# Kernel optimization log

Measured on AMD Instinct MI355X. Metric: run time of the kernel, lower is better.

Reference implementation:

```python
import jax, jax.numpy as jnp
import numpy as np

N_NODES = 200000
N_EDGES = 800000
N_MOL = 10000
IN_DIM, HDIM, EDGE_DIM = 40, 64, 16
BN_EPS = 1e-5


def _bn_eval(h, gamma, beta, mean, var):
    # BatchNorm1d in eval mode (running stats)
    return gamma * (h - mean) * jax.lax.rsqrt(var + BN_EPS) + beta


def _gine(x, src, dst, edge_attr, We, be, W, b, gamma, beta, mean, var):
    # GINEConv (eps=0): agg_i = sum_{(j->i)} relu(x_j + lin_e(e_ji)); h = nn(x + agg)
    msg = jax.nn.relu(x[src] + edge_attr @ We.T + be)          # [E, d]
    agg = jax.ops.segment_sum(msg, dst, num_segments=x.shape[0])
    h = (x + agg) @ W.T + b                                    # Linear
    h = _bn_eval(h, gamma, beta, mean, var)                    # BatchNorm1d
    return jax.nn.leaky_relu(h)                                # LeakyReLU(0.01); Dropout is identity in eval


def setup_inputs() -> dict:
    key = jax.random.key(0)
    ks = jax.random.split(key, 40)
    d = {}
    d['x'] = jax.random.normal(ks[0], (N_NODES, IN_DIM), jnp.float32)
    d['edge_index'] = jax.random.randint(ks[1], (2, N_EDGES), 0, N_NODES, jnp.int32)
    d['edge_attr'] = jax.random.normal(ks[2], (N_EDGES, EDGE_DIM), jnp.float32)
    d['batch'] = jnp.sort(jax.random.randint(ks[3], (N_NODES,), 0, N_MOL, jnp.int32))
    i = 4
    def nrm(shape, scale=0.05):
        nonlocal i
        i += 1
        return jax.random.normal(ks[i - 1], shape, jnp.float32) * scale
    for l, din in ((1, IN_DIM), (2, HDIM), (3, HDIM)):
        d[f'We{l}'] = nrm((din, EDGE_DIM)); d[f'be{l}'] = nrm((din,))
        d[f'W{l}'] = nrm((HDIM, din)); d[f'b{l}'] = nrm((HDIM,))
        d[f'g{l}'] = jnp.ones((HDIM,), jnp.float32); d[f'bb{l}'] = jnp.zeros((HDIM,), jnp.float32)
        d[f'm{l}'] = nrm((HDIM,)); d[f'v{l}'] = jax.random.uniform(ks[i], (HDIM,), jnp.float32, 0.5, 1.5); i += 1
    D4 = 4 * HDIM
    d['Wl1'] = nrm((D4, D4)); d['bl1'] = nrm((D4,))
    d['Wl2'] = nrm((1, D4)); d['bl2'] = nrm((1,))
    return d


def reference(x, edge_index, edge_attr, batch,
              We1, be1, W1, b1, g1, bb1, m1, v1,
              We2, be2, W2, b2, g2, bb2, m2, v2,
              We3, be3, W3, b3, g3, bb3, m3, v3,
              Wl1, bl1, Wl2, bl2):
    src, dst = edge_index[0], edge_index[1]
    h1 = _gine(x, src, dst, edge_attr, We1, be1, W1, b1, g1, bb1, m1, v1)
    h2 = _gine(h1, src, dst, edge_attr, We2, be2, W2, b2, g2, bb2, m2, v2)
    h3 = _gine(h2, src, dst, edge_attr, We3, be3, W3, b3, g3, bb3, m3, v3)
    h_pool = jax.ops.segment_sum(h3, batch, num_segments=N_MOL)   # global_add_pool
    h_pool_ = h_pool[batch]                                       # repeat_interleave by per-mol counts
    h = jnp.concatenate([h1, h2, h3, h_pool_], axis=1)            # [N, 4*hdim]
    h = jax.nn.leaky_relu(h @ Wl1.T + bl1)
    return h @ Wl2.T + bl2                                        # [N, 1]
```

## Files before the change

### kernel.cpp

```cpp
#include <hip/hip_runtime.h>
#include <hip/hip_bf16.h>

#define N_NODES 200000
#define N_EDGES 800000
#define N_MOL   10000
#define HDIM    64
#define EDGE_DIM 16
#define BN_EPS 1e-5f
#define SCAN_BLOCKS ((N_NODES + 255) / 256)

typedef __attribute__((ext_vector_type(8))) short short8;
typedef __attribute__((ext_vector_type(4))) float f32x4;

__device__ __forceinline__ unsigned int pk2(float a, float b) {
    __hip_bfloat162 h = __float22bfloat162_rn(make_float2(a, b));
    union { __hip_bfloat162 h; unsigned int u; } c;
    c.h = h;
    return c.u;
}
__device__ __forceinline__ short8 cvt8(float4 a, float4 b) {
    union { short8 s; unsigned int u[4]; } r;
    r.u[0] = pk2(a.x, a.y); r.u[1] = pk2(a.z, a.w);
    r.u[2] = pk2(b.x, b.y); r.u[3] = pk2(b.z, b.w);
    return r.s;
}
__device__ __forceinline__ float bf2f(unsigned short u) {
    return __uint_as_float(((unsigned int)u) << 16);
}

__global__ __launch_bounds__(256) void cvtx_kernel(
    const float* __restrict__ x, unsigned short* __restrict__ xb)
{
    int i = blockIdx.x * 256 + threadIdx.x;
    if ((size_t)i * 4 >= (size_t)N_NODES * 40) return;
    float4 v = *(const float4*)(x + (size_t)i * 4);
    union { ushort4 s; unsigned int u[2]; } r;
    r.u[0] = pk2(v.x, v.y); r.u[1] = pk2(v.z, v.w);
    *(ushort4*)(xb + (size_t)i * 4) = r.s;
}

__global__ __launch_bounds__(256) void hist_kernel(
    const int* __restrict__ ei, int* __restrict__ counts)
{
    int e = blockIdx.x * 256 + threadIdx.x;
    if (e < N_EDGES) atomicAdd(&counts[ei[N_EDGES + e]], 1);
}

__global__ __launch_bounds__(256) void scan_phase_a(
    const int* __restrict__ counts,
    int* __restrict__ row_ptr, int* __restrict__ block_sums)
{
    __shared__ int lds[256];
    int t = threadIdx.x;
    int i = blockIdx.x * 256 + t;
    int v = (i < N_NODES) ? counts[i] : 0;
    lds[t] = v;
    __syncthreads();
    for (int off = 1; off < 256; off <<= 1) {
        int u = (t >= off) ? lds[t - off] : 0;
        __syncthreads();
        lds[t] += u;
        __syncthreads();
    }
    if (i < N_NODES) row_ptr[i] = lds[t] - v;
    if (t == 255) block_sums[blockIdx.x] = lds[255];
}

__global__ __launch_bounds__(1024) void scan_phase_b(
    int* __restrict__ block_sums)
{
    __shared__ int lds[1024];
    int t = threadIdx.x;
    int v = (t < SCAN_BLOCKS) ? block_sums[t] : 0;
    lds[t] = v;
    __syncthreads();
    for (int off = 1; off < 1024; off <<= 1) {
        int u = (t >= off) ? lds[t - off] : 0;
        __syncthreads();
        lds[t] += u;
        __syncthreads();
    }
    if (t < SCAN_BLOCKS) block_sums[t] = lds[t] - v;
}

__global__ __launch_bounds__(256) void scan_phase_c(
    const int* __restrict__ block_sums,
    int* __restrict__ row_ptr, int* __restrict__ cursor)
{
    int i = blockIdx.x * 256 + threadIdx.x;
    if (i < N_NODES) {
        int v = row_ptr[i] + block_sums[blockIdx.x];
        row_ptr[i] = v;
        cursor[i] = v;
    }
    if (i == 0) row_ptr[N_NODES] = N_EDGES;
}

__global__ __launch_bounds__(256) void scatter_kernel(
    const int* __restrict__ ei, int* __restrict__ cursor,
    int* __restrict__ src_sorted, int* __restrict__ eid_sorted)
{
    int e = blockIdx.x * 256 + threadIdx.x;
    if (e >= N_EDGES) return;
    int d = ei[N_EDGES + e];
    int pos = atomicAdd(&cursor[d], 1);
    src_sorted[pos] = ei[e];
    eid_sorted[pos] = e;
}

template<int DIN>
__global__ __launch_bounds__(256) void agg_kernel(
    const unsigned short* __restrict__ feat,
    const int*   __restrict__ row_ptr,
    const int*   __restrict__ src_sorted,
    const int*   __restrict__ eid_sorted,
    const float* __restrict__ ea,
    const float* __restrict__ We,
    const float* __restrict__ be,
    float*       __restrict__ AGG)
{
    int lane = threadIdx.x & 63;
    int wv = __builtin_amdgcn_readfirstlane(blockIdx.x * 4 + (threadIdx.x >> 6));
    int n0 = wv * 8;
    if (n0 >= N_NODES) return;
    int f = lane;

    float wrow[16];
    float bias = 0.f;
    if (f < DIN) {
#pragma unroll
        for (int j = 0; j < 16; j++) wrow[j] = We[f * 16 + j];
        bias = be[f];
    } else {
#pragma unroll
        for (int j = 0; j < 16; j++) wrow[j] = 0.f;
    }

    int lo = row_ptr[n0];
    int hi = row_ptr[n0 + 8];
    int cur = 0;
    int nb = row_ptr[n0 + 1];
    float acc = 0.f;

    for (int j0 = lo; j0 < hi; j0 += 8) {
        int jn = min(8, hi - j0);
        int s[8], e[8];
#pragma unroll
        for (int k = 0; k < 8; k++) {
            int j = min(j0 + k, hi - 1);
            s[k] = src_sorted[j];
            e[k] = eid_sorted[j];
        }
        float xv[8];
#pragma unroll
        for (int k = 0; k < 8; k++)
            xv[k] = (f < DIN) ? bf2f(feat[(size_t)s[k] * DIN + f]) : 0.f;

#pragma unroll
        for (int k = 0; k < 8; k++) {
            if (k >= jn) break;
            int j = j0 + k;
            while (j >= nb) {
                float xd = (f < DIN) ? bf2f(feat[(size_t)(n0 + cur) * DIN + f]) : 0.f;
                AGG[(size_t)(n0 + cur) * HDIM + f] = acc + xd;
                acc = 0.f;
                cur++;
                nb = row_ptr[n0 + cur + 1];
            }
            const float4* ep = (const float4*)(ea + (size_t)e[k] * 16);
            float4 q0 = ep[0], q1 = ep[1], q2 = ep[2], q3 = ep[3];
            float a = bias;
            a = fmaf(q0.x, wrow[0],  a); a = fmaf(q0.y, wrow[1],  a);
            a = fmaf(q0.z, wrow[2],  a); a = fmaf(q0.w, wrow[3],  a);
            a = fmaf(q1.x, wrow[4],  a); a = fmaf(q1.y, wrow[5],  a);
            a = fmaf(q1.z, wrow[6],  a); a = fmaf(q1.w, wrow[7],  a);
            a = fmaf(q2.x, wrow[8],  a); a = fmaf(q2.y, wrow[9],  a);
            a = fmaf(q2.z, wrow[10], a); a = fmaf(q2.w, wrow[11], a);
            a = fmaf(q3.x, wrow[12], a); a = fmaf(q3.y, wrow[13], a);
            a = fmaf(q3.z, wrow[14], a); a = fmaf(q3.w, wrow[15], a);
            acc += fmaxf(xv[k] + a, 0.f);
        }
    }
    while (cur < 8) {
        float xd = (f < DIN) ? bf2f(feat[(size_t)(n0 + cur) * DIN + f]) : 0.f;
        AGG[(size_t)(n0 + cur) * HDIM + f] = acc + xd;
        acc = 0.f;
        cur++;
    }
}

template<int DIN>
__global__ __launch_bounds__(256) void node_mfma(
    const float*    __restrict__ AGG,
    unsigned short* __restrict__ Hb,
    const float* __restrict__ W,
    const float* __restrict__ bias,
    const float* __restrict__ gam,
    const float* __restrict__ bet,
    const float* __restrict__ mean,
    const float* __restrict__ var)
{
    int lane = threadIdx.x & 63;
    int wave = blockIdx.x * 4 + (threadIdx.x >> 6);
    if (wave >= N_NODES / 64) return;
    int n0 = wave * 64;
    int r = lane & 15;
    int g = lane >> 4;

    const short8 zero8 = (short8){0, 0, 0, 0, 0, 0, 0, 0};

    short8 zf[4][2];
#pragma unroll
    for (int nt = 0; nt < 4; nt++) {
        int node = n0 + nt * 16 + r;
        const float* ar = AGG + (size_t)node * HDIM;
        float4 a0 = *(const float4*)(ar + g * 8);
        float4 a1 = *(const float4*)(ar + g * 8 + 4);
        zf[nt][0] = cvt8(a0, a1);
        a0 = *(const float4*)(ar + 32 + g * 8);
        a1 = *(const float4*)(ar + 36 + g * 8);
        zf[nt][1] = cvt8(a0, a1);
    }

    const float4* b4  = (const float4*)bias;
    const float4* g4  = (const float4*)gam;
    const float4* be4 = (const float4*)bet;
    const float4* m4  = (const float4*)mean;
    const float4* v4  = (const float4*)var;

#pragma unroll
    for (int ft = 0; ft < 4; ft++) {
        const float* wr = W + (size_t)(ft * 16 + r) * DIN;
        short8 af[2];
        {
            float4 w0 = *(const float4*)(wr + g * 8);
            float4 w1 = *(const float4*)(wr + g * 8 + 4);
            af[0] = cvt8(w0, w1);
            if (DIN == 64) {
                w0 = *(const float4*)(wr + 32 + g * 8);
                w1 = *(const float4*)(wr + 36 + g * 8);
                af[1] = cvt8(w0, w1);
            } else if (g == 0) {
                w0 = *(const float4*)(wr + 32);
                w1 = *(const float4*)(wr + 36);
                af[1] = cvt8(w0, w1);
            } else {
                af[1] = zero8;
            }
        }

        f32x4 acc[4];
#pragma unroll
        for (int nt = 0; nt < 4; nt++) acc[nt] = (f32x4){0.f, 0.f, 0.f, 0.f};

#pragma unroll
        for (int ks = 0; ks < 2; ks++) {
#pragma unroll
            for (int nt = 0; nt < 4; nt++) {
                acc[nt] = __builtin_amdgcn_mfma_f32_16x16x32_bf16(
                    af[ks], zf[nt][ks], acc[nt], 0, 0, 0);
            }
        }

        int idx = ft * 4 + g;
        float4 bb = b4[idx], gg = g4[idx], bt = be4[idx], mm = m4[idx], vv = v4[idx];
        float s0 = gg.x * rsqrtf(vv.x + BN_EPS);
        float s1 = gg.y * rsqrtf(vv.y + BN_EPS);
        float s2 = gg.z * rsqrtf(vv.z + BN_EPS);
        float s3 = gg.w * rsqrtf(vv.w + BN_EPS);
#pragma unroll
        for (int nt = 0; nt < 4; nt++) {
            int node = n0 + nt * 16 + r;
            float y0 = s0 * (acc[nt][0] + bb.x - mm.x) + bt.x;
            float y1 = s1 * (acc[nt][1] + bb.y - mm.y) + bt.y;
            float y2 = s2 * (acc[nt][2] + bb.z - mm.z) + bt.z;
            float y3 = s3 * (acc[nt][3] + bb.w - mm.w) + bt.w;
            y0 = (y0 > 0.f) ? y0 : 0.01f * y0;
            y1 = (y1 > 0.f) ? y1 : 0.01f * y1;
            y2 = (y2 > 0.f) ? y2 : 0.01f * y2;
            y3 = (y3 > 0.f) ? y3 : 0.01f * y3;
            union { uint2 v; unsigned int u[2]; } st;
            st.u[0] = pk2(y0, y1);
            st.u[1] = pk2(y2, y3);
            *(uint2*)(Hb + (size_t)node * HDIM + ft * 16 + g * 4) = st.v;
        }
    }
}

__global__ __launch_bounds__(256) void pool_kernel(
    const unsigned short* __restrict__ h3b,
    const int*   __restrict__ batch,
    float*       __restrict__ hpool)
{
    int gid = blockIdx.x * 256 + threadIdx.x;
    if (gid >= N_NODES * HDIM) return;
    int i = gid >> 6, f = gid & 63;
    atomicAdd(&hpool[(size_t)batch[i] * HDIM + f], bf2f(h3b[gid]));
}

__global__ __launch_bounds__(256) void head_kernel(
    const unsigned short* __restrict__ h1b,
    const unsigned short* __restrict__ h2b,
    const unsigned short* __restrict__ h3b,
    const float* __restrict__ hpool,
    const int*   __restrict__ batch,
    const float* __restrict__ Wl1, const float* __restrict__ bl1,
    const float* __restrict__ Wl2, const float* __restrict__ bl2,
    float*       __restrict__ out)
{
    int lane = threadIdx.x & 63;
    int wave = blockIdx.x * 4 + (threadIdx.x >> 6);
    if (wave >= N_NODES / 64) return;
    int n0 = wave * 64;
    int r = lane & 15;
    int g = lane >> 4;

    short8 zf[4][8];
#pragma unroll
    for (int nt = 0; nt < 4; nt++) {
        int node = n0 + nt * 16 + r;
        const unsigned short* r1 = h1b + (size_t)node * 64;
        const unsigned short* r2 = h2b + (size_t)node * 64;
        const unsigned short* r3 = h3b + (size_t)node * 64;
        const float* rp = hpool + (size_t)batch[node] * 64;
        zf[nt][0] = *(const short8*)(r1 + g * 8);
        zf[nt][1] = *(const short8*)(r1 + 32 + g * 8);
        zf[nt][2] = *(const short8*)(r2 + g * 8);
        zf[nt][3] = *(const short8*)(r2 + 32 + g * 8);
        zf[nt][4] = *(const short8*)(r3 + g * 8);
        zf[nt][5] = *(const short8*)(r3 + 32 + g * 8);
        const float4* q;
        q = (const float4*)(rp + g * 8);        zf[nt][6] = cvt8(q[0], q[1]);
        q = (const float4*)(rp + 32 + g * 8);   zf[nt][7] = cvt8(q[0], q[1]);
    }

    float p[4] = {0.f, 0.f, 0.f, 0.f};

    const float4* bl1_4 = (const float4*)bl1;
    const float4* wl2_4 = (const float4*)Wl2;

#pragma unroll 1
    for (int ft = 0; ft < 16; ft++) {
        const float* arow = Wl1 + (size_t)(ft * 16 + r) * 256 + g * 8;
        short8 af[8];
#pragma unroll
        for (int ks = 0; ks < 8; ks++) {
            const float4* q = (const float4*)(arow + ks * 32);
            af[ks] = cvt8(q[0], q[1]);
        }

        f32x4 acc[4];
#pragma unroll
        for (int nt = 0; nt < 4; nt++) acc[nt] = (f32x4){0.f, 0.f, 0.f, 0.f};

#pragma unroll
        for (int ks = 0; ks < 8; ks++) {
#pragma unroll
            for (int nt = 0; nt < 4; nt++) {
                acc[nt] = __builtin_amdgcn_mfma_f32_16x16x32_bf16(
                    af[ks], zf[nt][ks], acc[nt], 0, 0, 0);
            }
        }

        float4 bl = bl1_4[ft * 4 + g];
        float4 w2 = wl2_4[ft * 4 + g];
#pragma unroll
        for (int nt = 0; nt < 4; nt++) {
            float a0 = acc[nt][0] + bl.x;
            float a1 = acc[nt][1] + bl.y;
            float a2 = acc[nt][2] + bl.z;
            float a3 = acc[nt][3] + bl.w;
            a0 = (a0 > 0.f) ? a0 : 0.01f * a0;
            a1 = (a1 > 0.f) ? a1 : 0.01f * a1;
            a2 = (a2 > 0.f) ? a2 : 0.01f * a2;
            a3 = (a3 > 0.f) ? a3 : 0.01f * a3;
            p[nt] += w2.x * a0 + w2.y * a1 + w2.z * a2 + w2.w * a3;
        }
    }

    float b2 = bl2[0];
#pragma unroll
    for (int nt = 0; nt < 4; nt++) {
        float s = p[nt];
        s += __shfl_xor(s, 16, 64);
        s += __shfl_xor(s, 32, 64);
        if (g == 0) out[n0 + nt * 16 + r] = s + b2;
    }
}

extern "C" void kernel_launch(void* const* d_in, const int* in_sizes, int n_in,
                              void* d_out, int out_size, void* d_ws, size_t ws_size,
                              hipStream_t stream) {
    const float* x     = (const float*)d_in[0];
    const int*   ei    = (const int*)  d_in[1];
    const float* ea    = (const float*)d_in[2];
    const int*   batch = (const int*)  d_in[3];

    const float* We1 = (const float*)d_in[4];  const float* be1 = (const float*)d_in[5];
    const float* W1  = (const float*)d_in[6];  const float* b1  = (const float*)d_in[7];
    const float* g1  = (const float*)d_in[8];  const float* bb1 = (const float*)d_in[9];
    const float* m1  = (const float*)d_in[10]; const float* v1  = (const float*)d_in[11];

    const float* We2 = (const float*)d_in[12]; const float* be2 = (const float*)d_in[13];
    const float* W2  = (const float*)d_in[14]; const float* b2  = (const float*)d_in[15];
    const float* g2  = (const float*)d_in[16]; const float* bb2 = (const float*)d_in[17];
    const float* m2  = (const float*)d_in[18]; const float* v2  = (const float*)d_in[19];

    const float* We3 = (const float*)d_in[20]; const float* be3 = (const float*)d_in[21];
    const float* W3  = (const float*)d_in[22]; const float* b3  = (const float*)d_in[23];
    const float* g3  = (const float*)d_in[24]; const float* bb3 = (const float*)d_in[25];
    const float* m3  = (const float*)d_in[26]; const float* v3  = (const float*)d_in[27];

    const float* Wl1 = (const float*)d_in[28]; const float* bl1 = (const float*)d_in[29];
    const float* Wl2 = (const float*)d_in[30]; const float* bl2 = (const float*)d_in[31];

    float* out = (float*)d_out;

    float* AGG            = (float*)d_ws;
    unsigned short* xb    = (unsigned short*)(AGG + (size_t)N_NODES * HDIM);
    unsigned short* Hb1   = xb + (size_t)N_NODES * 40;
    unsigned short* Hb2   = Hb1 + (size_t)N_NODES * HDIM;
    unsigned short* Hb3   = Hb2 + (size_t)N_NODES * HDIM;
    float* hpool          = (float*)(Hb3 + (size_t)N_NODES * HDIM);
    int* counts     = (int*)(hpool + (size_t)N_MOL * HDIM);
    int* row_ptr    = counts + N_NODES;
    int* cursor     = row_ptr + N_NODES + 1;
    int* src_sorted = cursor + N_NODES;
    int* eid_sorted = src_sorted + N_EDGES;
    int* block_sums = eid_sorted + N_EDGES;

    hipMemsetAsync(hpool, 0, (size_t)N_MOL * HDIM * sizeof(float), stream);
    hipMemsetAsync(counts, 0, (size_t)N_NODES * sizeof(int), stream);

    dim3 blk(256);
    dim3 cgrid(((size_t)N_NODES * 40 / 4 + 255) / 256);
    dim3 egrid(N_EDGES / 256);
    dim3 sgrid(SCAN_BLOCKS);
    dim3 agrid((N_NODES / 8) / 4);
    dim3 ngrid((N_NODES / 64 + 3) / 4);
    dim3 pgrid((N_NODES * HDIM) / 256);
    dim3 hgrid((N_NODES / 64 + 3) / 4);

    cvtx_kernel<<<cgrid, blk, 0, stream>>>(x, xb);
    hist_kernel<<<egrid, blk, 0, stream>>>(ei, counts);
    scan_phase_a<<<sgrid, blk, 0, stream>>>(counts, row_ptr, block_sums);
    scan_phase_b<<<1, 1024, 0, stream>>>(block_sums);
    scan_phase_c<<<sgrid, blk, 0, stream>>>(block_sums, row_ptr, cursor);
    scatter_kernel<<<egrid, blk, 0, stream>>>(ei, cursor, src_sorted, eid_sorted);

    agg_kernel<40><<<agrid, blk, 0, stream>>>(xb, row_ptr, src_sorted, eid_sorted,
                                              ea, We1, be1, AGG);
    node_mfma<40><<<ngrid, blk, 0, stream>>>(AGG, Hb1, W1, b1, g1, bb1, m1, v1);
    agg_kernel<64><<<agrid, blk, 0, stream>>>(Hb1, row_ptr, src_sorted, eid_sorted,
                                              ea, We2, be2, AGG);
    node_mfma<64><<<ngrid, blk, 0, stream>>>(AGG, Hb2, W2, b2, g2, bb2, m2, v2);
    agg_kernel<64><<<agrid, blk, 0, stream>>>(Hb2, row_ptr, src_sorted, eid_sorted,
                                              ea, We3, be3, AGG);
    node_mfma<64><<<ngrid, blk, 0, stream>>>(AGG, Hb3, W3, b3, g3, bb3, m3, v3);
    pool_kernel<<<pgrid, blk, 0, stream>>>(Hb3, batch, hpool);
    head_kernel<<<hgrid, blk, 0, stream>>>(Hb1, Hb2, Hb3, hpool, batch,
                                           Wl1, bl1, Wl2, bl2, out);
}
```

Measured before the change: 656.8 us.

## Precompute edge linear messages in dst-sorted bf16 buffer before aggregation

Adds a separate per-layer kernel that computes the edge-attribute linear transform (We·e + be) for every edge, ordered by destination-sorted position, and stores it as bf16. The aggregation kernel then streams these precomputed messages contiguously instead of gathering edge attributes by edge id and doing the 16-wide dot products inline. This trades inline compute and a random gather for an extra write and read of an E×DIN bf16 buffer per layer. The path is used only when the workspace is large enough, otherwise the old fused kernel runs.

```diff
diff --git a/kernel.cpp b/kernel.cpp
--- a/kernel.cpp
+++ b/kernel.cpp
@@ -106,6 +106,106 @@
     int pos = atomicAdd(&cursor[d], 1);
     src_sorted[pos] = ei[e];
     eid_sorted[pos] = e;
+}
+
+template<int DIN>
+__global__ __launch_bounds__(256) void emsg_kernel(
+    const float* __restrict__ ea,
+    const int*   __restrict__ eid_sorted,
+    const float* __restrict__ We,
+    const float* __restrict__ be,
+    unsigned short* __restrict__ emsg)
+{
+    constexpr int FPT = DIN / 4;
+    int tid = blockIdx.x * 256 + threadIdx.x;
+    int j = tid >> 2;
+    int q = tid & 3;
+    if (j >= N_EDGES) return;
+    int e = eid_sorted[j];
+    const float4* ep = (const float4*)(ea + (size_t)e * 16);
+    float4 a0 = ep[0], a1 = ep[1], a2 = ep[2], a3 = ep[3];
+
+    float vals[FPT];
+#pragma unroll
+    for (int i = 0; i < FPT; i++) {
+        int f = q * FPT + i;
+        const float4* w4 = (const float4*)(We + f * 16);
+        float4 w0 = w4[0], w1 = w4[1], w2 = w4[2], w3 = w4[3];
+        float a = be[f];
+        a += w0.x * a0.x + w0.y * a0.y + w0.z * a0.z + w0.w * a0.w;
+        a += w1.x * a1.x + w1.y * a1.y + w1.z * a1.z + w1.w * a1.w;
+        a += w2.x * a2.x + w2.y * a2.y + w2.z * a2.z + w2.w * a2.w;
+        a += w3.x * a3.x + w3.y * a3.y + w3.z * a3.z + w3.w * a3.w;
+        vals[i] = a;
+    }
+    unsigned short* orow = emsg + (size_t)j * DIN + q * FPT;
+    unsigned int u[FPT / 2];
+#pragma unroll
+    for (int i = 0; i < FPT / 2; i++) u[i] = pk2(vals[2 * i], vals[2 * i + 1]);
+    if constexpr (DIN == 64) {
+        uint4 s0 = make_uint4(u[0], u[1], u[2], u[3]);
+        uint4 s1 = make_uint4(u[4], u[5], u[6], u[7]);
+        *(uint4*)orow = s0;
+        *(uint4*)(orow + 8) = s1;
+    } else {
+#pragma unroll
+        for (int i = 0; i < FPT / 2; i++)
+            *((unsigned int*)orow + i) = u[i];
+    }
+}
+
+template<int DIN>
+__global__ __launch_bounds__(256) void agg_pre(
+    const unsigned short* __restrict__ feat,
+    const int*   __restrict__ row_ptr,
+    const int*   __restrict__ src_sorted,
+    const unsigned short* __restrict__ emsg,
+    float*       __restrict__ AGG)
+{
+    int lane = threadIdx.x & 63;
+    int wv = blockIdx.x * 4 + (threadIdx.x >> 6);
+    int n0 = wv * 8;
+    if (n0 >= N_NODES) return;
+    int f = lane;
+
+    int lo = row_ptr[n0];
+    int hi = row_ptr[n0 + 8];
+    int cur = 0;
+    int nb = row_ptr[n0 + 1];
+    float acc = 0.f;
+
+    for (int j0 = lo; j0 < hi; j0 += 8) {
+        int jn = min(8, hi - j0);
+        int s[8];
+#pragma unroll
+        for (int k = 0; k < 8; k++) s[k] = src_sorted[min(j0 + k, hi - 1)];
+        float xv[8], mv[8];
+#pragma unroll
+        for (int k = 0; k < 8; k++) {
+            int j = min(j0 + k, hi - 1);
+            xv[k] = (f < DIN) ? bf2f(feat[(size_t)s[k] * DIN + f]) : 0.f;
+            mv[k] = (f < DIN) ? bf2f(emsg[(size_t)j * DIN + f]) : 0.f;
+        }
+#pragma unroll
+        for (int k = 0; k < 8; k++) {
+            if (k >= jn) break;
+            int j = j0 + k;
+            while (j >= nb) {
+                float xd = (f < DIN) ? bf2f(feat[(size_t)(n0 + cur) * DIN + f]) : 0.f;
+                AGG[(size_t)(n0 + cur) * HDIM + f] = acc + xd;
+                acc = 0.f;
+                cur++;
+                nb = row_ptr[n0 + cur + 1];
+            }
+            acc += fmaxf(xv[k] + mv[k], 0.f);
+        }
+    }
+    while (cur < 8) {
+        float xd = (f < DIN) ? bf2f(feat[(size_t)(n0 + cur) * DIN + f]) : 0.f;
+        AGG[(size_t)(n0 + cur) * HDIM + f] = acc + xd;
+        acc = 0.f;
+        cur++;
+    }
 }
 
 template<int DIN>
@@ -428,6 +528,10 @@
     int* src_sorted = cursor + N_NODES;
     int* eid_sorted = src_sorted + N_EDGES;
     int* block_sums = eid_sorted + N_EDGES;
+    unsigned short* emsg  = (unsigned short*)(block_sums + SCAN_BLOCKS + 64);
+
+    size_t need = (size_t)((char*)(emsg + (size_t)N_EDGES * HDIM) - (char*)d_ws);
+    bool use_pre = (ws_size >= need);
 
     hipMemsetAsync(hpool, 0, (size_t)N_MOL * HDIM * sizeof(float), stream);
     hipMemsetAsync(counts, 0, (size_t)N_NODES * sizeof(int), stream);
@@ -435,6 +539,7 @@
     dim3 blk(256);
     dim3 cgrid(((size_t)N_NODES * 40 / 4 + 255) / 256);
     dim3 egrid(N_EDGES / 256);
+    dim3 mgrid((N_EDGES * 4) / 256);
     dim3 sgrid(SCAN_BLOCKS);
     dim3 agrid((N_NODES / 8) / 4);
     dim3 ngrid((N_NODES / 64 + 3) / 4);
@@ -448,15 +553,28 @@
     scan_phase_c<<<sgrid, blk, 0, stream>>>(block_sums, row_ptr, cursor);
     scatter_kernel<<<egrid, blk, 0, stream>>>(ei, cursor, src_sorted, eid_sorted);
 
-    agg_kernel<40><<<agrid, blk, 0, stream>>>(xb, row_ptr, src_sorted, eid_sorted,
-                                              ea, We1, be1, AGG);
-    node_mfma<40><<<ngrid, blk, 0, stream>>>(AGG, Hb1, W1, b1, g1, bb1, m1, v1);
-    agg_kernel<64><<<agrid, blk, 0, stream>>>(Hb1, row_ptr, src_sorted, eid_sorted,
-                                              ea, We2, be2, AGG);
-    node_mfma<64><<<ngrid, blk, 0, stream>>>(AGG, Hb2, W2, b2, g2, bb2, m2, v2);
-    agg_kernel<64><<<agrid, blk, 0, stream>>>(Hb2, row_ptr, src_sorted, eid_sorted,
-                                              ea, We3, be3, AGG);
-    node_mfma<64><<<ngrid, blk, 0, stream>>>(AGG, Hb3, W3, b3, g3, bb3, m3, v3);
+    if (use_pre) {
+        emsg_kernel<40><<<mgrid, blk, 0, stream>>>(ea, eid_sorted, We1, be1, emsg);
+        agg_pre<40><<<agrid, blk, 0, stream>>>(xb, row_ptr, src_sorted, emsg, AGG);
+        node_mfma<40><<<ngrid, blk, 0, stream>>>(AGG, Hb1, W1, b1, g1, bb1, m1, v1);
+        emsg_kernel<64><<<mgrid, blk, 0, stream>>>(ea, eid_sorted, We2, be2, emsg);
+        agg_pre<64><<<agrid, blk, 0, stream>>>(Hb1, row_ptr, src_sorted, emsg, AGG);
+        node_mfma<64><<<ngrid, blk, 0, stream>>>(AGG, Hb2, W2, b2, g2, bb2, m2, v2);
+        emsg_kernel<64><<<mgrid, blk, 0, stream>>>(ea, eid_sorted, We3, be3, emsg);
+        agg_pre<64><<<agrid, blk, 0, stream>>>(Hb2, row_ptr, src_sorted, emsg, AGG);
+        node_mfma<64><<<ngrid, blk, 0, stream>>>(AGG, Hb3, W3, b3, g3, bb3, m3, v3);
+    } else {
+        agg_kernel<40><<<agrid, blk, 0, stream>>>(xb, row_ptr, src_sorted, eid_sorted,
+                                                  ea, We1, be1, AGG);
+        node_mfma<40><<<ngrid, blk, 0, stream>>>(AGG, Hb1, W1, b1, g1, bb1, m1, v1);
+        agg_kernel<64><<<agrid, blk, 0, stream>>>(Hb1, row_ptr, src_sorted, eid_sorted,
+                                                  ea, We2, be2, AGG);
+        node_mfma<64><<<ngrid, blk, 0, stream>>>(AGG, Hb2, W2, b2, g2, bb2, m2, v2);
+        agg_kernel<64><<<agrid, blk, 0, stream>>>(Hb2, row_ptr, src_sorted, eid_sorted,
+                                                  ea, We3, be3, AGG);
+        node_mfma<64><<<ngrid, blk, 0, stream>>>(AGG, Hb3, W3, b3, g3, bb3, m3, v3);
+    }
+
     pool_kernel<<<pgrid, blk, 0, stream>>>(Hb3, batch, hpool);
     head_kernel<<<hgrid, blk, 0, stream>>>(Hb1, Hb2, Hb3, hpool, batch,
                                            Wl1, bl1, Wl2, bl2, out);
```

Result: slower. 1.546 ms (+135.5%).
